# Kernel optimization log

Hardware: AMD Instinct MI355X
Metric: run time of the kernel (lower is better)

The kernel has to match this reference:

```python
import jax, jax.numpy as jnp
import numpy as np

B = 8192          # batch (tokens)
D_IN = 4096       # in_features
D_OUT = 4096      # out_features
BS = 256          # block_size
K_IN = (D_IN + BS - 1) // BS
K_OUT = (D_OUT + BS - 1) // BS
INIT_SCALE = 0.1


def setup_inputs() -> dict:
    key = jax.random.key(0)
    k1, k2, k3, k4 = jax.random.split(key, 4)
    x = jax.random.normal(k1, (B, D_IN), dtype=jnp.float32)
    W = jax.random.normal(k2, (K_OUT, K_IN, BS), dtype=jnp.float32) * INIT_SCALE
    d_bernoulli = jnp.where(jax.random.bernoulli(k3, p=0.5, shape=(D_IN,)), 1.0, -1.0).astype(jnp.float32)
    bias = jax.random.normal(k4, (D_OUT,), dtype=jnp.float32) * INIT_SCALE
    return {"x": x, "W": W, "d_bernoulli": d_bernoulli, "bias": bias}


def _block_circulant_matmul(W, x, d):
    # W: (k_out, k_in, b); x: (batch, d_in); d: (d_in,) of +/-1
    batch = x.shape[0]
    k_out, k_in, b = W.shape
    x_d = x * d[None, :]
    pad_len = k_in * b - x.shape[-1]
    if pad_len > 0:
        x_d = jnp.pad(x_d, ((0, 0), (0, pad_len)))
    X_blocks = x_d.reshape(batch, k_in, b)          # (batch, k_in, b)
    X_fft = jnp.fft.fft(X_blocks, axis=-1)          # complex (batch, k_in, b)
    W_fft = jnp.fft.fft(W, axis=-1)                 # complex (k_out, k_in, b)
    # sum over k_in of X_fft * conj(W_fft[i]) for each output block i
    Y_fft = jnp.einsum('bjf,ijf->bif', X_fft, jnp.conjugate(W_fft))
    y = jnp.fft.ifft(Y_fft, axis=-1).real           # (batch, k_out, b)
    return y.reshape(batch, k_out * b)


def reference(x, W, d_bernoulli, bias):
    out = _block_circulant_matmul(W, x, d_bernoulli)
    out = out[..., :D_OUT]                          # truncate padded output blocks
    return out + bias[None, :]
```

## Files before the change

### kernel.cpp

```cpp
#include <hip/hip_runtime.h>


#define TWO_PI 6.283185307179586f
constexpr int RS = 304;
constexpr int RO = 16 * RS;

__device__ __forceinline__ int phys(int a) { return a + ((a >> 5) << 2); }

template<int SGN>
__device__ __forceinline__ void twmul(float& vr, float& vi, float c, float s)
{
    float r = vr * c + SGN * (vi * s);
    float i = vi * c - SGN * (vr * s);
    vr = r; vi = i;
}

template<int SGN, bool REAL>
__device__ __forceinline__ void pair1(float* __restrict__ Ar, float* __restrict__ Ai,
                                      int base, int u)
{
    float xr[2][16], xi[2][16];
#pragma unroll
    for (int r = 0; r < 2; ++r)
#pragma unroll
        for (int s = 0; s < 16; ++s) {
            int a = base + r * RO + phys(u + 16 * s);
            xr[r][s] = Ar[a];
            if (!REAL) xi[r][s] = Ai[a];
        }
    float su, cu;
    __sincosf((float)u * (TWO_PI / 256.f), &su, &cu);
    const float CM[4] = {1.f, 0.92387953f, 0.70710678f, 0.38268343f};
    const float SM[4] = {0.f, 0.38268343f, 0.70710678f, 0.92387953f};
    float c1[4], s1[4], c2[4], s2[4], c3[4], s3[4];
#pragma unroll
    for (int m = 0; m < 4; ++m) {
        c1[m] = cu * CM[m] - su * SM[m];
        s1[m] = su * CM[m] + cu * SM[m];
        c2[m] = c1[m] * c1[m] - s1[m] * s1[m];
        s2[m] = 2.f * c1[m] * s1[m];
        c3[m] = c2[m] * c1[m] - s2[m] * s1[m];
        s3[m] = s2[m] * c1[m] + c2[m] * s1[m];
    }
    float cb1 = cu * cu - su * su, sb1 = 2.f * cu * su;
    { float c = cb1, s = sb1; cb1 = c * c - s * s; sb1 = 2.f * c * s; }
    float cb2 = cb1 * cb1 - sb1 * sb1, sb2 = 2.f * cb1 * sb1;
    float cb3 = cb2 * cb1 - sb2 * sb1, sb3 = sb2 * cb1 + cb2 * sb1;

#pragma unroll
    for (int r = 0; r < 2; ++r) {
#pragma unroll
        for (int m = 0; m < 4; ++m) {
            if (REAL) {
                float a0 = xr[r][m], a1 = xr[r][m + 4], a2 = xr[r][m + 8], a3 = xr[r][m + 12];
                float t0 = a0 + a2, t1 = a0 - a2, t2 = a1 + a3, t3 = a1 - a3;
                xr[r][m] = t0 + t2;  xi[r][m] = 0.f;
                xr[r][m + 4]  = t1 * c1[m] - t3 * s1[m];
                xi[r][m + 4]  = -SGN * (t3 * c1[m] + t1 * s1[m]);
                float dd      = t0 - t2;
                xr[r][m + 8]  = dd * c2[m];
                xi[r][m + 8]  = -SGN * (dd * s2[m]);
                xr[r][m + 12] = t1 * c3[m] + t3 * s3[m];
                xi[r][m + 12] = SGN * (t3 * c3[m] - t1 * s3[m]);
            } else {
                float t0r = xr[r][m] + xr[r][m + 8],       t0i = xi[r][m] + xi[r][m + 8];
                float t1r = xr[r][m] - xr[r][m + 8],       t1i = xi[r][m] - xi[r][m + 8];
                float t2r = xr[r][m + 4] + xr[r][m + 12],  t2i = xi[r][m + 4] + xi[r][m + 12];
                float t3r = xr[r][m + 4] - xr[r][m + 12],  t3i = xi[r][m + 4] - xi[r][m + 12];
                xr[r][m] = t0r + t2r;  xi[r][m] = t0i + t2i;
                float v1r = t1r + SGN * t3i, v1i = t1i - SGN * t3r;
                float v2r = t0r - t2r,       v2i = t0i - t2i;
                float v3r = t1r - SGN * t3i, v3i = t1i + SGN * t3r;
                twmul<SGN>(v1r, v1i, c1[m], s1[m]);
                twmul<SGN>(v2r, v2i, c2[m], s2[m]);
                twmul<SGN>(v3r, v3i, c3[m], s3[m]);
                xr[r][m + 4]  = v1r; xi[r][m + 4]  = v1i;
                xr[r][m + 8]  = v2r; xi[r][m + 8]  = v2i;
                xr[r][m + 12] = v3r; xi[r][m + 12] = v3i;
            }
        }
#pragma unroll
        for (int k = 0; k < 4; ++k) {
            int s0 = 4 * k;
            float t0r = xr[r][s0] + xr[r][s0 + 2],     t0i = xi[r][s0] + xi[r][s0 + 2];
            float t1r = xr[r][s0] - xr[r][s0 + 2],     t1i = xi[r][s0] - xi[r][s0 + 2];
            float t2r = xr[r][s0 + 1] + xr[r][s0 + 3], t2i = xi[r][s0 + 1] + xi[r][s0 + 3];
            float t3r = xr[r][s0 + 1] - xr[r][s0 + 3], t3i = xi[r][s0 + 1] - xi[r][s0 + 3];
            xr[r][s0] = t0r + t2r;  xi[r][s0] = t0i + t2i;
            float v1r = t1r + SGN * t3i, v1i = t1i - SGN * t3r;
            float v2r = t0r - t2r,       v2i = t0i - t2i;
            float v3r = t1r - SGN * t3i, v3i = t1i + SGN * t3r;
            twmul<SGN>(v1r, v1i, cb1, sb1);
            twmul<SGN>(v2r, v2i, cb2, sb2);
            twmul<SGN>(v3r, v3i, cb3, sb3);
            xr[r][s0 + 1] = v1r; xi[r][s0 + 1] = v1i;
            xr[r][s0 + 2] = v2r; xi[r][s0 + 2] = v2i;
            xr[r][s0 + 3] = v3r; xi[r][s0 + 3] = v3i;
        }
    }
#pragma unroll
    for (int r = 0; r < 2; ++r)
#pragma unroll
        for (int s = 0; s < 16; ++s) {
            int a = base + r * RO + phys(u + 16 * s);
            Ar[a] = xr[r][s]; Ai[a] = xi[r][s];
        }
}

template<int SGN, bool STORE_REV, bool REAL_OUT>
__device__ __forceinline__ void pair2(float* __restrict__ Ar, float* __restrict__ Ai,
                                      int base, int u)
{
    int a0 = base + 16 * u + ((u >> 1) << 2);
    float xr[2][16], xi[2][16];
#pragma unroll
    for (int r = 0; r < 2; ++r)
#pragma unroll
        for (int v = 0; v < 4; ++v) {
            float4 vr = *(const float4*)(Ar + a0 + r * RO + 4 * v);
            float4 vi = *(const float4*)(Ai + a0 + r * RO + 4 * v);
            xr[r][4 * v] = vr.x; xr[r][4 * v + 1] = vr.y; xr[r][4 * v + 2] = vr.z; xr[r][4 * v + 3] = vr.w;
            xi[r][4 * v] = vi.x; xi[r][4 * v + 1] = vi.y; xi[r][4 * v + 2] = vi.z; xi[r][4 * v + 3] = vi.w;
        }
    const float CQ[4][4] = {
        {1.f, 1.f, 1.f, 1.f},
        {1.f, 0.92387953f, 0.70710678f, 0.38268343f},
        {1.f, 0.70710678f, 0.f, -0.70710678f},
        {1.f, 0.38268343f, -0.70710678f, -0.92387953f}};
    const float SQ[4][4] = {
        {0.f, 0.f, 0.f, 0.f},
        {0.f, 0.38268343f, 0.70710678f, 0.92387953f},
        {0.f, 0.70710678f, 1.f, 0.70710678f},
        {0.f, 0.92387953f, 0.70710678f, -0.38268343f}};
#pragma unroll
    for (int r = 0; r < 2; ++r) {
#pragma unroll
        for (int q = 0; q < 4; ++q) {
            float t0r = xr[r][q] + xr[r][q + 8],       t0i = xi[r][q] + xi[r][q + 8];
            float t1r = xr[r][q] - xr[r][q + 8],       t1i = xi[r][q] - xi[r][q + 8];
            float t2r = xr[r][q + 4] + xr[r][q + 12],  t2i = xi[r][q + 4] + xi[r][q + 12];
            float t3r = xr[r][q + 4] - xr[r][q + 12],  t3i = xi[r][q + 4] - xi[r][q + 12];
            xr[r][q] = t0r + t2r;  xi[r][q] = t0i + t2i;
            float v1r = t1r + SGN * t3i, v1i = t1i - SGN * t3r;
            float v2r = t0r - t2r,       v2i = t0i - t2i;
            float v3r = t1r - SGN * t3i, v3i = t1i + SGN * t3r;
            twmul<SGN>(v1r, v1i, CQ[q][1], SQ[q][1]);
            twmul<SGN>(v2r, v2i, CQ[q][2], SQ[q][2]);
            twmul<SGN>(v3r, v3i, CQ[q][3], SQ[q][3]);
            xr[r][q + 4]  = v1r; xi[r][q + 4]  = v1i;
            xr[r][q + 8]  = v2r; xi[r][q + 8]  = v2i;
            xr[r][q + 12] = v3r; xi[r][q + 12] = v3i;
        }
#pragma unroll
        for (int g = 0; g < 4; ++g) {
            int s0 = 4 * g;
            float t0r = xr[r][s0] + xr[r][s0 + 2],     t1r = xr[r][s0] - xr[r][s0 + 2];
            float t2r = xr[r][s0 + 1] + xr[r][s0 + 3], t3r = xr[r][s0 + 1] - xr[r][s0 + 3];
            float t0i = xi[r][s0] + xi[r][s0 + 2],     t1i = xi[r][s0] - xi[r][s0 + 2];
            float t2i = xi[r][s0 + 1] + xi[r][s0 + 3], t3i = xi[r][s0 + 1] - xi[r][s0 + 3];
            xr[r][s0]     = t0r + t2r;
            xr[r][s0 + 1] = t1r + SGN * t3i;
            xr[r][s0 + 2] = t0r - t2r;
            xr[r][s0 + 3] = t1r - SGN * t3i;
            if (!REAL_OUT) {
                xi[r][s0]     = t0i + t2i;
                xi[r][s0 + 1] = t1i - SGN * t3r;
                xi[r][s0 + 2] = t0i - t2i;
                xi[r][s0 + 3] = t1i + SGN * t3r;
            }
        }
    }
    if (STORE_REV) {
        int q2 = (u >> 2) + ((u & 3) << 2);
#pragma unroll
        for (int r = 0; r < 2; ++r)
#pragma unroll
            for (int s = 0; s < 16; ++s) {
                int dest = q2 + ((s >> 2) << 4) + ((s & 3) << 6);
                int a = base + r * RO + phys(dest);
                Ar[a] = xr[r][s]; Ai[a] = xi[r][s];
            }
    } else {
#pragma unroll
        for (int r = 0; r < 2; ++r)
#pragma unroll
            for (int v = 0; v < 4; ++v) {
                *(float4*)(Ar + a0 + r * RO + 4 * v) =
                    make_float4(xr[r][4*v], xr[r][4*v+1], xr[r][4*v+2], xr[r][4*v+3]);
                if (!REAL_OUT)
                    *(float4*)(Ai + a0 + r * RO + 4 * v) =
                        make_float4(xi[r][4*v], xi[r][4*v+1], xi[r][4*v+2], xi[r][4*v+3]);
            }
    }
}

__global__ __launch_bounds__(256) void wfft_kernel(const float* __restrict__ W,
                                                   float* __restrict__ Wc4)
{
    __shared__ float wblk[256];
    __shared__ float tabc[256], tabs[256];
    int t   = threadIdx.x;
    int blk = blockIdx.x;
    wblk[t] = W[blk * 256 + t];
    float s, c;
    __sincosf((float)t * (TWO_PI / 256.f), &s, &c);
    tabc[t] = c; tabs[t] = s;
    __syncthreads();
    if (t <= 128) {
        float ar = 0.f, ai = 0.f;
        for (int cc = 0; cc < 256; ++cc) {
            int idx = (t * cc) & 255;
            float wv = wblk[cc];
            ar = fmaf(wv, tabc[idx], ar);
            ai = fmaf(wv, tabs[idx], ai);
        }
        int i = blk >> 4, j = blk & 15;
        int flat = ((i * 8 + (j >> 1)) * 132 + t) * 4 + ((j & 1) << 1);
        Wc4[flat]     = ar;
        Wc4[flat + 1] = ai;
    }
}

__global__ __launch_bounds__(256, 2) void bc_kernel(const float* __restrict__ x,
                                                    const float* __restrict__ d,
                                                    const float* __restrict__ bias,
                                                    const float* __restrict__ Wc4,
                                                    float* __restrict__ out)
{
    __shared__ float Ar[2 * 16 * RS], Ai[2 * 16 * RS];
    int t  = threadIdx.x;
    int b0 = blockIdx.x * 2;
    int w = t >> 6, l = t & 63;
    int u = t & 15;
    int base = (t >> 4) * RS;

    const float4* d4 = (const float4*)d;
#pragma unroll
    for (int it = 0; it < 4; ++it) {
        int idx = 256 * w + 64 * it + l;
        float4 dv = d4[idx];
        int a = (4 * w + it) * RS + 4 * l + ((l >> 3) << 2);
#pragma unroll
        for (int r = 0; r < 2; ++r) {
            float4 xv = ((const float4*)(x + (size_t)(b0 + r) * 4096))[idx];
            *(float4*)(Ar + a + r * RO) =
                make_float4(xv.x * dv.x, xv.y * dv.y, xv.z * dv.z, xv.w * dv.w);
        }
    }

    pair1<1, true>(Ar, Ai, base, u);
    pair2<1, true, false>(Ar, Ai, base, u);
    __syncthreads();

    {
        int f  = t & 127;
        int pf = phys(f);
        float vr[2][16], vi[2][16];
#pragma unroll
        for (int r = 0; r < 2; ++r)
#pragma unroll
            for (int j = 0; j < 16; ++j) {
                vr[r][j] = Ar[r * RO + j * RS + pf];
                vi[r][j] = Ai[r * RO + j * RS + pf];
            }
        bool x128 = (t >= 64 && t < 80);
        int p8 = phys(128);
        float v8r[2][16], v8i[2][16];
        if (x128) {
#pragma unroll
            for (int r = 0; r < 2; ++r)
#pragma unroll
                for (int j = 0; j < 16; ++j) {
                    v8r[r][j] = Ar[r * RO + j * RS + p8];
                    v8i[r][j] = Ai[r * RO + j * RS + p8];
                }
        }
        __syncthreads();
        const float4* wb = (const float4*)Wc4;
        int ib = (t >> 7) * 8;
#pragma unroll
        for (int io = 0; io < 8; ++io) {
            int i = ib + io;
            float yr0 = 0.f, yi0 = 0.f, yr1 = 0.f, yi1 = 0.f;
#pragma unroll
            for (int jc = 0; jc < 8; ++jc) {
                float4 wv = wb[(i * 8 + jc) * 132 + f];
                int j0 = 2 * jc;
                yr0 = fmaf(vr[0][j0], wv.x, yr0); yr0 = fmaf(-vi[0][j0], wv.y, yr0);
                yi0 = fmaf(vr[0][j0], wv.y, yi0); yi0 = fmaf(vi[0][j0], wv.x, yi0);
                yr0 = fmaf(vr[0][j0+1], wv.z, yr0); yr0 = fmaf(-vi[0][j0+1], wv.w, yr0);
                yi0 = fmaf(vr[0][j0+1], wv.w, yi0); yi0 = fmaf(vi[0][j0+1], wv.z, yi0);
                yr1 = fmaf(vr[1][j0], wv.x, yr1); yr1 = fmaf(-vi[1][j0], wv.y, yr1);
                yi1 = fmaf(vr[1][j0], wv.y, yi1); yi1 = fmaf(vi[1][j0], wv.x, yi1);
                yr1 = fmaf(vr[1][j0+1], wv.z, yr1); yr1 = fmaf(-vi[1][j0+1], wv.w, yr1);
                yi1 = fmaf(vr[1][j0+1], wv.w, yi1); yi1 = fmaf(vi[1][j0+1], wv.z, yi1);
            }
            Ar[i * RS + pf] = yr0;        Ai[i * RS + pf] = yi0;
            Ar[RO + i * RS + pf] = yr1;   Ai[RO + i * RS + pf] = yi1;
            if (f >= 1) {
                int pc = phys(256 - f);
                Ar[i * RS + pc] = yr0;       Ai[i * RS + pc] = -yi0;
                Ar[RO + i * RS + pc] = yr1;  Ai[RO + i * RS + pc] = -yi1;
            }
        }
        if (x128) {
            int i = t - 64;
#pragma unroll
            for (int r = 0; r < 2; ++r) {
                float yr = 0.f, yi = 0.f;
#pragma unroll
                for (int jc = 0; jc < 8; ++jc) {
                    float4 wv = wb[(i * 8 + jc) * 132 + 128];
                    int j0 = 2 * jc;
                    yr = fmaf(v8r[r][j0], wv.x, yr); yr = fmaf(-v8i[r][j0], wv.y, yr);
                    yi = fmaf(v8r[r][j0], wv.y, yi); yi = fmaf(v8i[r][j0], wv.x, yi);
                    yr = fmaf(v8r[r][j0+1], wv.z, yr); yr = fmaf(-v8i[r][j0+1], wv.w, yr);
                    yi = fmaf(v8r[r][j0+1], wv.w, yi); yi = fmaf(v8i[r][j0+1], wv.z, yi);
                }
                Ar[r * RO + i * RS + p8] = yr;
                Ai[r * RO + i * RS + p8] = yi;
            }
        }
    }
    __syncthreads();

    pair1<-1, false>(Ar, Ai, base, u);
    pair2<-1, false, true>(Ar, Ai, base, u);

    const float4* b4 = (const float4*)bias;
    int dbase = ((l >> 4) & 3) + (((l >> 2) & 3) << 2) + ((l & 3) << 4);
#pragma unroll
    for (int it = 0; it < 4; ++it) {
        int idx = 256 * w + 64 * it + l;
        int rb  = (4 * w + it) * RS;
        float4 bv = b4[idx];
#pragma unroll
        for (int r = 0; r < 2; ++r) {
            float vv[4];
#pragma unroll
            for (int e = 0; e < 4; ++e) {
                int dest = dbase + (e << 6);
                vv[e] = Ar[r * RO + rb + phys(dest)];
            }
            float4 ov;
            ov.x = vv[0] * (1.f / 256.f) + bv.x;
            ov.y = vv[1] * (1.f / 256.f) + bv.y;
            ov.z = vv[2] * (1.f / 256.f) + bv.z;
            ov.w = vv[3] * (1.f / 256.f) + bv.w;
            ((float4*)(out + (size_t)(b0 + r) * 4096))[idx] = ov;
        }
    }
}

extern "C" void kernel_launch(void* const* d_in, const int* in_sizes, int n_in,
                              void* d_out, int out_size, void* d_ws, size_t ws_size,
                              hipStream_t stream)
{
    const float* x    = (const float*)d_in[0];
    const float* W    = (const float*)d_in[1];
    const float* d    = (const float*)d_in[2];
    const float* bias = (const float*)d_in[3];
    float* out = (float*)d_out;
    float* Wc4 = (float*)d_ws;

    wfft_kernel<<<256, 256, 0, stream>>>(W, Wc4);
    bc_kernel<<<4096, 256, 0, stream>>>(x, d, bias, Wc4, out);
}
```

Baseline: 300.2 us.

## Pack two real rows into one complex FFT to halve shared memory and FFT work

Uses the two-for-one real FFT trick: the two batch rows are loaded as the real and imaginary parts of a single complex signal, so only one complex forward and one inverse FFT run per block instead of two half-real ones. The spectra are separated using conjugate-symmetric bins, multiplied by the W spectrum, and recombined so the inverse FFT returns both rows in its real and imaginary parts. Shared memory per block is halved, which lets the launch bound rise to 4 blocks per CU. In exchange each thread reads the mirrored bins as well, and the changed scaling (1/512) and pairing logic add some risk to numerical correctness.

```diff
diff --git a/kernel.cpp b/kernel.cpp
--- a/kernel.cpp
+++ b/kernel.cpp
@@ -3,7 +3,6 @@
 
 #define TWO_PI 6.283185307179586f
 constexpr int RS = 304;
-constexpr int RO = 16 * RS;
 
 __device__ __forceinline__ int phys(int a) { return a + ((a >> 5) << 2); }
 
@@ -15,19 +14,17 @@
     vr = r; vi = i;
 }
 
-template<int SGN, bool REAL>
+template<int SGN>
 __device__ __forceinline__ void pair1(float* __restrict__ Ar, float* __restrict__ Ai,
                                       int base, int u)
 {
-    float xr[2][16], xi[2][16];
-#pragma unroll
-    for (int r = 0; r < 2; ++r)
-#pragma unroll
-        for (int s = 0; s < 16; ++s) {
-            int a = base + r * RO + phys(u + 16 * s);
-            xr[r][s] = Ar[a];
-            if (!REAL) xi[r][s] = Ai[a];
-        }
+    float xr[16], xi[16];
+#pragma unroll
+    for (int s = 0; s < 16; ++s) {
+        int a = base + phys(u + 16 * s);
+        xr[s] = Ar[a];
+        xi[s] = Ai[a];
+    }
     float su, cu;
     __sincosf((float)u * (TWO_PI / 256.f), &su, &cu);
     const float CM[4] = {1.f, 0.92387953f, 0.70710678f, 0.38268343f};
@@ -42,86 +39,65 @@
         c3[m] = c2[m] * c1[m] - s2[m] * s1[m];
         s3[m] = s2[m] * c1[m] + c2[m] * s1[m];
     }
+#pragma unroll
+    for (int m = 0; m < 4; ++m) {
+        float t0r = xr[m] + xr[m + 8],       t0i = xi[m] + xi[m + 8];
+        float t1r = xr[m] - xr[m + 8],       t1i = xi[m] - xi[m + 8];
+        float t2r = xr[m + 4] + xr[m + 12],  t2i = xi[m + 4] + xi[m + 12];
+        float t3r = xr[m + 4] - xr[m + 12],  t3i = xi[m + 4] - xi[m + 12];
+        xr[m] = t0r + t2r;  xi[m] = t0i + t2i;
+        float v1r = t1r + SGN * t3i, v1i = t1i - SGN * t3r;
+        float v2r = t0r - t2r,       v2i = t0i - t2i;
+        float v3r = t1r - SGN * t3i, v3i = t1i + SGN * t3r;
+        twmul<SGN>(v1r, v1i, c1[m], s1[m]);
+        twmul<SGN>(v2r, v2i, c2[m], s2[m]);
+        twmul<SGN>(v3r, v3i, c3[m], s3[m]);
+        xr[m + 4]  = v1r; xi[m + 4]  = v1i;
+        xr[m + 8]  = v2r; xi[m + 8]  = v2i;
+        xr[m + 12] = v3r; xi[m + 12] = v3i;
+    }
     float cb1 = cu * cu - su * su, sb1 = 2.f * cu * su;
     { float c = cb1, s = sb1; cb1 = c * c - s * s; sb1 = 2.f * c * s; }
     float cb2 = cb1 * cb1 - sb1 * sb1, sb2 = 2.f * cb1 * sb1;
     float cb3 = cb2 * cb1 - sb2 * sb1, sb3 = sb2 * cb1 + cb2 * sb1;
-
-#pragma unroll
-    for (int r = 0; r < 2; ++r) {
-#pragma unroll
-        for (int m = 0; m < 4; ++m) {
-            if (REAL) {
-                float a0 = xr[r][m], a1 = xr[r][m + 4], a2 = xr[r][m + 8], a3 = xr[r][m + 12];
-                float t0 = a0 + a2, t1 = a0 - a2, t2 = a1 + a3, t3 = a1 - a3;
-                xr[r][m] = t0 + t2;  xi[r][m] = 0.f;
-                xr[r][m + 4]  = t1 * c1[m] - t3 * s1[m];
-                xi[r][m + 4]  = -SGN * (t3 * c1[m] + t1 * s1[m]);
-                float dd      = t0 - t2;
-                xr[r][m + 8]  = dd * c2[m];
-                xi[r][m + 8]  = -SGN * (dd * s2[m]);
-                xr[r][m + 12] = t1 * c3[m] + t3 * s3[m];
-                xi[r][m + 12] = SGN * (t3 * c3[m] - t1 * s3[m]);
-            } else {
-                float t0r = xr[r][m] + xr[r][m + 8],       t0i = xi[r][m] + xi[r][m + 8];
-                float t1r = xr[r][m] - xr[r][m + 8],       t1i = xi[r][m] - xi[r][m + 8];
-                float t2r = xr[r][m + 4] + xr[r][m + 12],  t2i = xi[r][m + 4] + xi[r][m + 12];
-                float t3r = xr[r][m + 4] - xr[r][m + 12],  t3i = xi[r][m + 4] - xi[r][m + 12];
-                xr[r][m] = t0r + t2r;  xi[r][m] = t0i + t2i;
-                float v1r = t1r + SGN * t3i, v1i = t1i - SGN * t3r;
-                float v2r = t0r - t2r,       v2i = t0i - t2i;
-                float v3r = t1r - SGN * t3i, v3i = t1i + SGN * t3r;
-                twmul<SGN>(v1r, v1i, c1[m], s1[m]);
-                twmul<SGN>(v2r, v2i, c2[m], s2[m]);
-                twmul<SGN>(v3r, v3i, c3[m], s3[m]);
-                xr[r][m + 4]  = v1r; xi[r][m + 4]  = v1i;
-                xr[r][m + 8]  = v2r; xi[r][m + 8]  = v2i;
-                xr[r][m + 12] = v3r; xi[r][m + 12] = v3i;
-            }
-        }
-#pragma unroll
-        for (int k = 0; k < 4; ++k) {
-            int s0 = 4 * k;
-            float t0r = xr[r][s0] + xr[r][s0 + 2],     t0i = xi[r][s0] + xi[r][s0 + 2];
-            float t1r = xr[r][s0] - xr[r][s0 + 2],     t1i = xi[r][s0] - xi[r][s0 + 2];
-            float t2r = xr[r][s0 + 1] + xr[r][s0 + 3], t2i = xi[r][s0 + 1] + xi[r][s0 + 3];
-            float t3r = xr[r][s0 + 1] - xr[r][s0 + 3], t3i = xi[r][s0 + 1] - xi[r][s0 + 3];
-            xr[r][s0] = t0r + t2r;  xi[r][s0] = t0i + t2i;
-            float v1r = t1r + SGN * t3i, v1i = t1i - SGN * t3r;
-            float v2r = t0r - t2r,       v2i = t0i - t2i;
-            float v3r = t1r - SGN * t3i, v3i = t1i + SGN * t3r;
-            twmul<SGN>(v1r, v1i, cb1, sb1);
-            twmul<SGN>(v2r, v2i, cb2, sb2);
-            twmul<SGN>(v3r, v3i, cb3, sb3);
-            xr[r][s0 + 1] = v1r; xi[r][s0 + 1] = v1i;
-            xr[r][s0 + 2] = v2r; xi[r][s0 + 2] = v2i;
-            xr[r][s0 + 3] = v3r; xi[r][s0 + 3] = v3i;
-        }
-    }
-#pragma unroll
-    for (int r = 0; r < 2; ++r)
-#pragma unroll
-        for (int s = 0; s < 16; ++s) {
-            int a = base + r * RO + phys(u + 16 * s);
-            Ar[a] = xr[r][s]; Ai[a] = xi[r][s];
-        }
-}
-
-template<int SGN, bool STORE_REV, bool REAL_OUT>
+#pragma unroll
+    for (int k = 0; k < 4; ++k) {
+        int s0 = 4 * k;
+        float t0r = xr[s0] + xr[s0 + 2],     t0i = xi[s0] + xi[s0 + 2];
+        float t1r = xr[s0] - xr[s0 + 2],     t1i = xi[s0] - xi[s0 + 2];
+        float t2r = xr[s0 + 1] + xr[s0 + 3], t2i = xi[s0 + 1] + xi[s0 + 3];
+        float t3r = xr[s0 + 1] - xr[s0 + 3], t3i = xi[s0 + 1] - xi[s0 + 3];
+        xr[s0] = t0r + t2r;  xi[s0] = t0i + t2i;
+        float v1r = t1r + SGN * t3i, v1i = t1i - SGN * t3r;
+        float v2r = t0r - t2r,       v2i = t0i - t2i;
+        float v3r = t1r - SGN * t3i, v3i = t1i + SGN * t3r;
+        twmul<SGN>(v1r, v1i, cb1, sb1);
+        twmul<SGN>(v2r, v2i, cb2, sb2);
+        twmul<SGN>(v3r, v3i, cb3, sb3);
+        xr[s0 + 1] = v1r; xi[s0 + 1] = v1i;
+        xr[s0 + 2] = v2r; xi[s0 + 2] = v2i;
+        xr[s0 + 3] = v3r; xi[s0 + 3] = v3i;
+    }
+#pragma unroll
+    for (int s = 0; s < 16; ++s) {
+        int a = base + phys(u + 16 * s);
+        Ar[a] = xr[s]; Ai[a] = xi[s];
+    }
+}
+
+template<int SGN, bool STORE_REV>
 __device__ __forceinline__ void pair2(float* __restrict__ Ar, float* __restrict__ Ai,
                                       int base, int u)
 {
     int a0 = base + 16 * u + ((u >> 1) << 2);
-    float xr[2][16], xi[2][16];
-#pragma unroll
-    for (int r = 0; r < 2; ++r)
-#pragma unroll
-        for (int v = 0; v < 4; ++v) {
-            float4 vr = *(const float4*)(Ar + a0 + r * RO + 4 * v);
-            float4 vi = *(const float4*)(Ai + a0 + r * RO + 4 * v);
-            xr[r][4 * v] = vr.x; xr[r][4 * v + 1] = vr.y; xr[r][4 * v + 2] = vr.z; xr[r][4 * v + 3] = vr.w;
-            xi[r][4 * v] = vi.x; xi[r][4 * v + 1] = vi.y; xi[r][4 * v + 2] = vi.z; xi[r][4 * v + 3] = vi.w;
-        }
+    float xr[16], xi[16];
+#pragma unroll
+    for (int v = 0; v < 4; ++v) {
+        float4 vr = *(const float4*)(Ar + a0 + 4 * v);
+        float4 vi = *(const float4*)(Ai + a0 + 4 * v);
+        xr[4 * v] = vr.x; xr[4 * v + 1] = vr.y; xr[4 * v + 2] = vr.z; xr[4 * v + 3] = vr.w;
+        xi[4 * v] = vi.x; xi[4 * v + 1] = vi.y; xi[4 * v + 2] = vi.z; xi[4 * v + 3] = vi.w;
+    }
     const float CQ[4][4] = {
         {1.f, 1.f, 1.f, 1.f},
         {1.f, 0.92387953f, 0.70710678f, 0.38268343f},
@@ -133,64 +109,48 @@
         {0.f, 0.70710678f, 1.f, 0.70710678f},
         {0.f, 0.92387953f, 0.70710678f, -0.38268343f}};
 #pragma unroll
-    for (int r = 0; r < 2; ++r) {
-#pragma unroll
-        for (int q = 0; q < 4; ++q) {
-            float t0r = xr[r][q] + xr[r][q + 8],       t0i = xi[r][q] + xi[r][q + 8];
-            float t1r = xr[r][q] - xr[r][q + 8],       t1i = xi[r][q] - xi[r][q + 8];
-            float t2r = xr[r][q + 4] + xr[r][q + 12],  t2i = xi[r][q + 4] + xi[r][q + 12];
-            float t3r = xr[r][q + 4] - xr[r][q + 12],  t3i = xi[r][q + 4] - xi[r][q + 12];
-            xr[r][q] = t0r + t2r;  xi[r][q] = t0i + t2i;
-            float v1r = t1r + SGN * t3i, v1i = t1i - SGN * t3r;
-            float v2r = t0r - t2r,       v2i = t0i - t2i;
-            float v3r = t1r - SGN * t3i, v3i = t1i + SGN * t3r;
-            twmul<SGN>(v1r, v1i, CQ[q][1], SQ[q][1]);
-            twmul<SGN>(v2r, v2i, CQ[q][2], SQ[q][2]);
-            twmul<SGN>(v3r, v3i, CQ[q][3], SQ[q][3]);
-            xr[r][q + 4]  = v1r; xi[r][q + 4]  = v1i;
-            xr[r][q + 8]  = v2r; xi[r][q + 8]  = v2i;
-            xr[r][q + 12] = v3r; xi[r][q + 12] = v3i;
-        }
-#pragma unroll
-        for (int g = 0; g < 4; ++g) {
-            int s0 = 4 * g;
-            float t0r = xr[r][s0] + xr[r][s0 + 2],     t1r = xr[r][s0] - xr[r][s0 + 2];
-            float t2r = xr[r][s0 + 1] + xr[r][s0 + 3], t3r = xr[r][s0 + 1] - xr[r][s0 + 3];
-            float t0i = xi[r][s0] + xi[r][s0 + 2],     t1i = xi[r][s0] - xi[r][s0 + 2];
-            float t2i = xi[r][s0 + 1] + xi[r][s0 + 3], t3i = xi[r][s0 + 1] - xi[r][s0 + 3];
-            xr[r][s0]     = t0r + t2r;
-            xr[r][s0 + 1] = t1r + SGN * t3i;
-            xr[r][s0 + 2] = t0r - t2r;
-            xr[r][s0 + 3] = t1r - SGN * t3i;
-            if (!REAL_OUT) {
-                xi[r][s0]     = t0i + t2i;
-                xi[r][s0 + 1] = t1i - SGN * t3r;
-                xi[r][s0 + 2] = t0i - t2i;
-                xi[r][s0 + 3] = t1i + SGN * t3r;
-            }
-        }
+    for (int q = 0; q < 4; ++q) {
+        float t0r = xr[q] + xr[q + 8],       t0i = xi[q] + xi[q + 8];
+        float t1r = xr[q] - xr[q + 8],       t1i = xi[q] - xi[q + 8];
+        float t2r = xr[q + 4] + xr[q + 12],  t2i = xi[q + 4] + xi[q + 12];
+        float t3r = xr[q + 4] - xr[q + 12],  t3i = xi[q + 4] - xi[q + 12];
+        xr[q] = t0r + t2r;  xi[q] = t0i + t2i;
+        float v1r = t1r + SGN * t3i, v1i = t1i - SGN * t3r;
+        float v2r = t0r - t2r,       v2i = t0i - t2i;
+        float v3r = t1r - SGN * t3i, v3i = t1i + SGN * t3r;
+        twmul<SGN>(v1r, v1i, CQ[q][1], SQ[q][1]);
+        twmul<SGN>(v2r, v2i, CQ[q][2], SQ[q][2]);
+        twmul<SGN>(v3r, v3i, CQ[q][3], SQ[q][3]);
+        xr[q + 4]  = v1r; xi[q + 4]  = v1i;
+        xr[q + 8]  = v2r; xi[q + 8]  = v2i;
+        xr[q + 12] = v3r; xi[q + 12] = v3i;
+    }
+#pragma unroll
+    for (int g = 0; g < 4; ++g) {
+        int s0 = 4 * g;
+        float t0r = xr[s0] + xr[s0 + 2],     t1r = xr[s0] - xr[s0 + 2];
+        float t2r = xr[s0 + 1] + xr[s0 + 3], t3r = xr[s0 + 1] - xr[s0 + 3];
+        float t0i = xi[s0] + xi[s0 + 2],     t1i = xi[s0] - xi[s0 + 2];
+        float t2i = xi[s0 + 1] + xi[s0 + 3], t3i = xi[s0 + 1] - xi[s0 + 3];
+        xr[s0]     = t0r + t2r;  xi[s0]     = t0i + t2i;
+        xr[s0 + 1] = t1r + SGN * t3i;  xi[s0 + 1] = t1i - SGN * t3r;
+        xr[s0 + 2] = t0r - t2r;        xi[s0 + 2] = t0i - t2i;
+        xr[s0 + 3] = t1r - SGN * t3i;  xi[s0 + 3] = t1i + SGN * t3r;
     }
     if (STORE_REV) {
         int q2 = (u >> 2) + ((u & 3) << 2);
 #pragma unroll
-        for (int r = 0; r < 2; ++r)
-#pragma unroll
-            for (int s = 0; s < 16; ++s) {
-                int dest = q2 + ((s >> 2) << 4) + ((s & 3) << 6);
-                int a = base + r * RO + phys(dest);
-                Ar[a] = xr[r][s]; Ai[a] = xi[r][s];
-            }
+        for (int s = 0; s < 16; ++s) {
+            int dest = q2 + ((s >> 2) << 4) + ((s & 3) << 6);
+            int a = base + phys(dest);
+            Ar[a] = xr[s]; Ai[a] = xi[s];
+        }
     } else {
 #pragma unroll
-        for (int r = 0; r < 2; ++r)
-#pragma unroll
-            for (int v = 0; v < 4; ++v) {
-                *(float4*)(Ar + a0 + r * RO + 4 * v) =
-                    make_float4(xr[r][4*v], xr[r][4*v+1], xr[r][4*v+2], xr[r][4*v+3]);
-                if (!REAL_OUT)
-                    *(float4*)(Ai + a0 + r * RO + 4 * v) =
-                        make_float4(xi[r][4*v], xi[r][4*v+1], xi[r][4*v+2], xi[r][4*v+3]);
-            }
+        for (int v = 0; v < 4; ++v) {
+            *(float4*)(Ar + a0 + 4 * v) = make_float4(xr[4*v], xr[4*v+1], xr[4*v+2], xr[4*v+3]);
+            *(float4*)(Ai + a0 + 4 * v) = make_float4(xi[4*v], xi[4*v+1], xi[4*v+2], xi[4*v+3]);
+        }
     }
 }
 
@@ -221,13 +181,13 @@
     }
 }
 
-__global__ __launch_bounds__(256, 2) void bc_kernel(const float* __restrict__ x,
+__global__ __launch_bounds__(256, 4) void bc_kernel(const float* __restrict__ x,
                                                     const float* __restrict__ d,
                                                     const float* __restrict__ bias,
                                                     const float* __restrict__ Wc4,
                                                     float* __restrict__ out)
 {
-    __shared__ float Ar[2 * 16 * RS], Ai[2 * 16 * RS];
+    __shared__ float Ar[16 * RS], Ai[16 * RS];
     int t  = threadIdx.x;
     int b0 = blockIdx.x * 2;
     int w = t >> 6, l = t & 63;
@@ -235,47 +195,53 @@
     int base = (t >> 4) * RS;
 
     const float4* d4 = (const float4*)d;
+    const float4* x40 = (const float4*)(x + (size_t)b0 * 4096);
+    const float4* x41 = (const float4*)(x + (size_t)(b0 + 1) * 4096);
 #pragma unroll
     for (int it = 0; it < 4; ++it) {
         int idx = 256 * w + 64 * it + l;
         float4 dv = d4[idx];
+        float4 v0 = x40[idx];
+        float4 v1 = x41[idx];
         int a = (4 * w + it) * RS + 4 * l + ((l >> 3) << 2);
-#pragma unroll
-        for (int r = 0; r < 2; ++r) {
-            float4 xv = ((const float4*)(x + (size_t)(b0 + r) * 4096))[idx];
-            *(float4*)(Ar + a + r * RO) =
-                make_float4(xv.x * dv.x, xv.y * dv.y, xv.z * dv.z, xv.w * dv.w);
-        }
-    }
-
-    pair1<1, true>(Ar, Ai, base, u);
-    pair2<1, true, false>(Ar, Ai, base, u);
+        *(float4*)(Ar + a) = make_float4(v0.x * dv.x, v0.y * dv.y, v0.z * dv.z, v0.w * dv.w);
+        *(float4*)(Ai + a) = make_float4(v1.x * dv.x, v1.y * dv.y, v1.z * dv.z, v1.w * dv.w);
+    }
+
+    pair1<1>(Ar, Ai, base, u);
+    pair2<1, true>(Ar, Ai, base, u);
     __syncthreads();
 
     {
         int f  = t & 127;
         int pf = phys(f);
-        float vr[2][16], vi[2][16];
-#pragma unroll
-        for (int r = 0; r < 2; ++r)
-#pragma unroll
-            for (int j = 0; j < 16; ++j) {
-                vr[r][j] = Ar[r * RO + j * RS + pf];
-                vi[r][j] = Ai[r * RO + j * RS + pf];
-            }
+        int pc = phys((256 - f) & 255);
+        float zr[16], zi[16], z2r[16], z2i[16];
+#pragma unroll
+        for (int j = 0; j < 16; ++j) {
+            zr[j]  = Ar[j * RS + pf];  zi[j]  = Ai[j * RS + pf];
+            z2r[j] = Ar[j * RS + pc];  z2i[j] = Ai[j * RS + pc];
+        }
         bool x128 = (t >= 64 && t < 80);
         int p8 = phys(128);
-        float v8r[2][16], v8i[2][16];
+        float z8r[16], z8i[16];
         if (x128) {
 #pragma unroll
-            for (int r = 0; r < 2; ++r)
-#pragma unroll
-                for (int j = 0; j < 16; ++j) {
-                    v8r[r][j] = Ar[r * RO + j * RS + p8];
-                    v8i[r][j] = Ai[r * RO + j * RS + p8];
-                }
+            for (int j = 0; j < 16; ++j) {
+                z8r[j] = Ar[j * RS + p8];
+                z8i[j] = Ai[j * RS + p8];
+            }
         }
         __syncthreads();
+
+#pragma unroll
+        for (int j = 0; j < 16; ++j) {
+            float a = zr[j], b = zi[j], c = z2r[j], dd = z2i[j];
+            zr[j]  = a + c;
+            zi[j]  = b - dd;
+            z2r[j] = b + dd;
+            z2i[j] = c - a;
+        }
         const float4* wb = (const float4*)Wc4;
         int ib = (t >> 7) * 8;
 #pragma unroll
@@ -286,69 +252,70 @@
             for (int jc = 0; jc < 8; ++jc) {
                 float4 wv = wb[(i * 8 + jc) * 132 + f];
                 int j0 = 2 * jc;
-                yr0 = fmaf(vr[0][j0], wv.x, yr0); yr0 = fmaf(-vi[0][j0], wv.y, yr0);
-                yi0 = fmaf(vr[0][j0], wv.y, yi0); yi0 = fmaf(vi[0][j0], wv.x, yi0);
-                yr0 = fmaf(vr[0][j0+1], wv.z, yr0); yr0 = fmaf(-vi[0][j0+1], wv.w, yr0);
-                yi0 = fmaf(vr[0][j0+1], wv.w, yi0); yi0 = fmaf(vi[0][j0+1], wv.z, yi0);
-                yr1 = fmaf(vr[1][j0], wv.x, yr1); yr1 = fmaf(-vi[1][j0], wv.y, yr1);
-                yi1 = fmaf(vr[1][j0], wv.y, yi1); yi1 = fmaf(vi[1][j0], wv.x, yi1);
-                yr1 = fmaf(vr[1][j0+1], wv.z, yr1); yr1 = fmaf(-vi[1][j0+1], wv.w, yr1);
-                yi1 = fmaf(vr[1][j0+1], wv.w, yi1); yi1 = fmaf(vi[1][j0+1], wv.z, yi1);
+                yr0 = fmaf(zr[j0], wv.x, yr0);  yr0 = fmaf(-zi[j0], wv.y, yr0);
+                yi0 = fmaf(zr[j0], wv.y, yi0);  yi0 = fmaf(zi[j0], wv.x, yi0);
+                yr1 = fmaf(z2r[j0], wv.x, yr1); yr1 = fmaf(-z2i[j0], wv.y, yr1);
+                yi1 = fmaf(z2r[j0], wv.y, yi1); yi1 = fmaf(z2i[j0], wv.x, yi1);
+                yr0 = fmaf(zr[j0+1], wv.z, yr0);  yr0 = fmaf(-zi[j0+1], wv.w, yr0);
+                yi0 = fmaf(zr[j0+1], wv.w, yi0);  yi0 = fmaf(zi[j0+1], wv.z, yi0);
+                yr1 = fmaf(z2r[j0+1], wv.z, yr1); yr1 = fmaf(-z2i[j0+1], wv.w, yr1);
+                yi1 = fmaf(z2r[j0+1], wv.w, yi1); yi1 = fmaf(z2i[j0+1], wv.z, yi1);
             }
-            Ar[i * RS + pf] = yr0;        Ai[i * RS + pf] = yi0;
-            Ar[RO + i * RS + pf] = yr1;   Ai[RO + i * RS + pf] = yi1;
+            Ar[i * RS + pf] = yr0 - yi1;
+            Ai[i * RS + pf] = yi0 + yr1;
             if (f >= 1) {
-                int pc = phys(256 - f);
-                Ar[i * RS + pc] = yr0;       Ai[i * RS + pc] = -yi0;
-                Ar[RO + i * RS + pc] = yr1;  Ai[RO + i * RS + pc] = -yi1;
+                Ar[i * RS + pc] = yr0 + yi1;
+                Ai[i * RS + pc] = yr1 - yi0;
             }
         }
         if (x128) {
             int i = t - 64;
-#pragma unroll
-            for (int r = 0; r < 2; ++r) {
-                float yr = 0.f, yi = 0.f;
-#pragma unroll
-                for (int jc = 0; jc < 8; ++jc) {
-                    float4 wv = wb[(i * 8 + jc) * 132 + 128];
-                    int j0 = 2 * jc;
-                    yr = fmaf(v8r[r][j0], wv.x, yr); yr = fmaf(-v8i[r][j0], wv.y, yr);
-                    yi = fmaf(v8r[r][j0], wv.y, yi); yi = fmaf(v8i[r][j0], wv.x, yi);
-                    yr = fmaf(v8r[r][j0+1], wv.z, yr); yr = fmaf(-v8i[r][j0+1], wv.w, yr);
-                    yi = fmaf(v8r[r][j0+1], wv.w, yi); yi = fmaf(v8i[r][j0+1], wv.z, yi);
-                }
-                Ar[r * RO + i * RS + p8] = yr;
-                Ai[r * RO + i * RS + p8] = yi;
+            float yr0 = 0.f, yi0 = 0.f, yr1 = 0.f, yi1 = 0.f;
+#pragma unroll
+            for (int jc = 0; jc < 8; ++jc) {
+                float4 wv = wb[(i * 8 + jc) * 132 + 128];
+                int j0 = 2 * jc;
+                yr0 = fmaf(z8r[j0], wv.x, yr0);   yi0 = fmaf(z8r[j0], wv.y, yi0);
+                yr1 = fmaf(z8i[j0], wv.x, yr1);   yi1 = fmaf(z8i[j0], wv.y, yi1);
+                yr0 = fmaf(z8r[j0+1], wv.z, yr0); yi0 = fmaf(z8r[j0+1], wv.w, yi0);
+                yr1 = fmaf(z8i[j0+1], wv.z, yr1); yi1 = fmaf(z8i[j0+1], wv.w, yi1);
             }
+            Ar[i * RS + p8] = 2.f * (yr0 - yi1);
+            Ai[i * RS + p8] = 2.f * (yi0 + yr1);
         }
     }
     __syncthreads();
 
-    pair1<-1, false>(Ar, Ai, base, u);
-    pair2<-1, false, true>(Ar, Ai, base, u);
+    pair1<-1>(Ar, Ai, base, u);
+    pair2<-1, false>(Ar, Ai, base, u);
 
     const float4* b4 = (const float4*)bias;
+    float* o0 = out + (size_t)b0 * 4096;
+    float* o1 = out + (size_t)(b0 + 1) * 4096;
     int dbase = ((l >> 4) & 3) + (((l >> 2) & 3) << 2) + ((l & 3) << 4);
 #pragma unroll
     for (int it = 0; it < 4; ++it) {
         int idx = 256 * w + 64 * it + l;
         int rb  = (4 * w + it) * RS;
+        float v0[4], v1[4];
+#pragma unroll
+        for (int e = 0; e < 4; ++e) {
+            int a = rb + phys(dbase + (e << 6));
+            v0[e] = Ar[a];
+            v1[e] = Ai[a];
+        }
         float4 bv = b4[idx];
-#pragma unroll
-        for (int r = 0; r < 2; ++r) {
-            float vv[4];
-#pragma unroll
-            for (int e = 0; e < 4; ++e) {
-                int dest = dbase + (e << 6);
-                vv[e] = Ar[r * RO + rb + phys(dest)];
-            }
-            float4 ov;
-            ov.x = vv[0] * (1.f / 256.f) + bv.x;
-            ov.y = vv[1] * (1.f / 256.f) + bv.y;
-            ov.z = vv[2] * (1.f / 256.f) + bv.z;
-            ov.w = vv[3] * (1.f / 256.f) + bv.w;
-            ((float4*)(out + (size_t)(b0 + r) * 4096))[idx] = ov;
-        }
+        float4 ov0, ov1;
+        ov0.x = v0[0] * (1.f / 512.f) + bv.x;
+        ov0.y = v0[1] * (1.f / 512.f) + bv.y;
+        ov0.z = v0[2] * (1.f / 512.f) + bv.z;
+        ov0.w = v0[3] * (1.f / 512.f) + bv.w;
+        ov1.x = v1[0] * (1.f / 512.f) + bv.x;
+        ov1.y = v1[1] * (1.f / 512.f) + bv.y;
+        ov1.z = v1[2] * (1.f / 512.f) + bv.z;
+        ov1.w = v1[3] * (1.f / 512.f) + bv.w;
+        ((float4*)o0)[idx] = ov0;
+        ((float4*)o1)[idx] = ov1;
     }
 }
 
```

Result: slower. 379.3 us (+26.4%).
